# Kernel optimization log

Hardware: AMD Instinct MI355X
Metric: run time of the kernel (lower is better)

The kernel has to match this reference:

```python
import jax, jax.numpy as jnp
import numpy as np


def _rope(xh, theta_factor):
    # xh: [H, S, Dqk]; rotate first half against second half (as in source)
    S, D = xh.shape[-2], xh.shape[-1]
    d_rope = D // 2
    rate = theta_factor * (-jnp.arange(0, d_rope, dtype=xh.dtype) / d_rope)
    pos = jnp.arange(0, S, dtype=xh.dtype)
    rot = pos[:, None] * rate[None, :]            # [S, d_rope]
    sin, cos = jnp.sin(rot), jnp.cos(rot)
    x1, x2 = xh[..., :d_rope], xh[..., d_rope:]
    y1 = cos * x1 - sin * x2
    y2 = sin * x1 + cos * x2
    return jnp.concatenate([y1, y2], axis=-1)


def _mha(x, y, q, k, v, o, theta_factor):
    S = x.shape[0]
    d_model = x.shape[1]
    x_scale = 1.0 / jnp.sqrt(jnp.array(x.shape[1], x.dtype))
    y_scale = 1.0 / jnp.sqrt(jnp.array(y.shape[1], x.dtype))
    # causal additive mask: 0 on/below diagonal, -1e9 above
    mask = (jnp.tril(jnp.ones((S, S), x.dtype)) - 1.0) * 1000000000.0
    # per-head projections (note: source uses x_scale for both q and k)
    pre_q = jnp.einsum('sd,hdk->hsk', x, q) * x_scale
    pre_k = jnp.einsum('td,hdk->htk', y, k) * x_scale
    vs = jnp.einsum('td,hdv->htv', y, v) * y_scale
    rq = _rope(pre_q, theta_factor)
    rk = _rope(pre_k, theta_factor)
    attn_scale = 1.0 / jnp.sqrt(jnp.array(rq.shape[-1], x.dtype))
    scores = jnp.einsum('hsk,htk->hst', rq, rk) * attn_scale + mask
    w = jax.nn.softmax(scores, axis=-1)           # [H, S, S]
    z = jnp.einsum('hst,htv->hsv', w, vs)         # [H, S, Dv]
    out_scale = 1.0 / jnp.sqrt(jnp.array(o.shape[0] * o.shape[1], x.dtype))
    return jnp.einsum('hsv,hvd->sd', z, o) * out_scale


def setup_inputs() -> dict:
    key = jax.random.key(0)
    ks = jax.random.split(key, 5)
    S, D, H, Dqk, Dv = 2048, 2048, 16, 128, 128
    return {
        'x': jax.random.normal(ks[0], (S, D), jnp.float32),
        'q': jax.random.normal(ks[1], (H, D, Dqk), jnp.float32),
        'k': jax.random.normal(ks[2], (H, D, Dqk), jnp.float32),
        'v': jax.random.normal(ks[3], (H, D, Dv), jnp.float32),
        'o': jax.random.normal(ks[4], (H, Dv, D), jnp.float32),
        'theta_factor': jnp.array(10000.0, jnp.float32),
    }


def reference(x, q, k, v, o, theta_factor):
    # self-attention path (y = x), scale = 1
    return _mha(x, x, q, k, v, o, theta_factor)
```

## Files before the change

kernel.cpp:

```cpp
#include <hip/hip_runtime.h>


#define S_LEN   2048
#define D_MODEL 2048
#define NHEAD   16
#define DHEAD   128

using f32x4   = __attribute__((ext_vector_type(4))) float;
using f32x16  = __attribute__((ext_vector_type(16))) float;
using bf16x8  = __attribute__((ext_vector_type(8))) __bf16;

__device__ __forceinline__ unsigned short f2bf(float f) {
  unsigned int u = __builtin_bit_cast(unsigned int, f);
  u += 0x7fffu + ((u >> 16) & 1u);
  return (unsigned short)(u >> 16);
}
__device__ __forceinline__ int chunks_of(int qt) { return (4 * qt + 13) / 10; }

__device__ __forceinline__ void gl_lds16(const unsigned short* g, char* l) {
  __builtin_amdgcn_global_load_lds(
      (const __attribute__((address_space(1))) unsigned int*)g,
      (__attribute__((address_space(3))) unsigned int*)l, 16, 0, 0);
}

__global__ void k_cvt(const float* __restrict__ in, unsigned short* __restrict__ out) {
  int i = (blockIdx.x * 256 + threadIdx.x) * 4;
  float4 v = *reinterpret_cast<const float4*>(in + i);
  ushort4 o; o.x = f2bf(v.x); o.y = f2bf(v.y); o.z = f2bf(v.z); o.w = f2bf(v.w);
  *reinterpret_cast<ushort4*>(out + i) = o;
}

__global__ void k_tab(const float* __restrict__ theta_p, float* __restrict__ sint,
                      float* __restrict__ cost) {
  int i = blockIdx.x * 256 + threadIdx.x;
  int s = i >> 6, c = i & 63;
  float rate = theta_p[0] * (-(float)c / 64.0f);
  float sn, cs;
  sincosf((float)s * rate, &sn, &cs);
  sint[i] = sn; cost[i] = cs;
}

__global__ void k_tr(const float* __restrict__ in, unsigned short* __restrict__ out,
                     int R, int C) {
  __shared__ float t[32][33];
  int b = blockIdx.x, rt = blockIdx.y, ct = blockIdx.z;
  const float* ip = in + (size_t)b * R * C;
  unsigned short* op = out + (size_t)b * R * C;
  int tx = threadIdx.x & 31, ty = threadIdx.x >> 5;
  #pragma unroll
  for (int i = 0; i < 4; i++)
    t[ty + i * 8][tx] = ip[(size_t)(rt * 32 + ty + i * 8) * C + ct * 32 + tx];
  __syncthreads();
  #pragma unroll
  for (int i = 0; i < 4; i++)
    op[(size_t)(ct * 32 + ty + i * 8) * R + rt * 32 + tx] = f2bf(t[tx][ty + i * 8]);
}

__global__ __launch_bounds__(256) void k_proj2(
    const unsigned short* __restrict__ xb, const unsigned short* __restrict__ wT,
    const float* __restrict__ sint, const float* __restrict__ cost,
    unsigned short* __restrict__ rq, unsigned short* __restrict__ rk,
    unsigned short* __restrict__ vst) {
  __shared__ char lds[65536];
  const int tid = threadIdx.x, l = tid & 63, w = tid >> 6;
  const int lr = l & 15, lk = l >> 4;
  const int orig = blockIdx.x;
  const int wg = (orig & 7) * 96 + (orig >> 3);
  const int bx = wg & 15, by = wg >> 4;
  const int s0 = bx * 128;
  const int h = by & 15, which = by >> 4;
  const unsigned short* bbase = wT + (size_t)by * 128 * D_MODEL;

  f32x4 acc[2][8] = {};

  auto stage = [&](int t, int buf) {
    const int kt = t * 64;
    char* dst = lds + buf * 32768;
    #pragma unroll
    for (int j = 0; j < 4; j++) {
      int ci = (j * 4 + w) * 64 + l;
      int r = ci >> 3, c8 = ci & 7;
      int csrc = (c8 ^ (r & 7)) * 8;
      gl_lds16(xb + (size_t)(s0 + r) * D_MODEL + kt + csrc, dst + ci * 16);
      gl_lds16(bbase + (size_t)r * D_MODEL + kt + csrc, dst + 16384 + ci * 16);
    }
  };

  stage(0, 0);
  int cur = 0;
  const int nT = D_MODEL / 64;
  for (int t = 0; t < nT; t++) {
    if (t + 1 < nT) {
      stage(t + 1, cur ^ 1);
      asm volatile("s_waitcnt vmcnt(8)" ::: "memory");
    } else {
      asm volatile("s_waitcnt vmcnt(0)" ::: "memory");
    }
    __builtin_amdgcn_s_barrier();
    const char* base = lds + cur * 32768;
    #pragma unroll
    for (int kk = 0; kk < 2; kk++) {
      const int kb = kk * 64 + lk * 16;
      bf16x8 a[2], b[8];
      #pragma unroll
      for (int mf = 0; mf < 2; mf++) {
        int rr = w * 32 + mf * 16 + lr;
        a[mf] = *reinterpret_cast<const bf16x8*>(base + rr * 128 + (kb ^ ((rr & 7) << 4)));
      }
      #pragma unroll
      for (int nf = 0; nf < 8; nf++) {
        int rn = nf * 16 + lr;
        b[nf] = *reinterpret_cast<const bf16x8*>(base + 16384 + rn * 128 + (kb ^ ((rn & 7) << 4)));
      }
      #pragma unroll
      for (int mf = 0; mf < 2; mf++)
        #pragma unroll
        for (int nf = 0; nf < 8; nf++)
          acc[mf][nf] = __builtin_amdgcn_mfma_f32_16x16x32_bf16(a[mf], b[nf], acc[mf][nf], 0, 0, 0);
    }
    asm volatile("s_waitcnt lgkmcnt(0)" ::: "memory");
    __builtin_amdgcn_s_barrier();
    cur ^= 1;
  }

  const float xscale = 0.022097086912079608f;
  const float qsc = xscale * 0.08838834764831845f;
  if (which < 2) {
    const float sc_out = (which == 0) ? qsc : xscale;
    unsigned short* dst = (which == 0 ? rq : rk) + (size_t)h * S_LEN * DHEAD;
    #pragma unroll
    for (int mf = 0; mf < 2; mf++) {
      #pragma unroll
      for (int nf = 0; nf < 4; nf++) {
        int c1 = nf * 16 + lr;
        #pragma unroll
        for (int rg = 0; rg < 4; rg++) {
          int srow = s0 + w * 32 + mf * 16 + lk * 4 + rg;
          float sn = sint[srow * 64 + c1], cs = cost[srow * 64 + c1];
          float x1 = acc[mf][nf][rg] * sc_out;
          float x2 = acc[mf][nf + 4][rg] * sc_out;
          dst[(size_t)srow * DHEAD + c1]      = f2bf(cs * x1 - sn * x2);
          dst[(size_t)srow * DHEAD + c1 + 64] = f2bf(sn * x1 + cs * x2);
        }
      }
    }
  } else {
    unsigned short* dst = vst + (size_t)h * DHEAD * S_LEN;
    #pragma unroll
    for (int mf = 0; mf < 2; mf++) {
      int rbase = s0 + w * 32 + mf * 16 + lk * 4;
      #pragma unroll
      for (int nf = 0; nf < 8; nf++) {
        int c = nf * 16 + lr;
        ushort4 ov;
        ov.x = f2bf(acc[mf][nf][0] * xscale); ov.y = f2bf(acc[mf][nf][1] * xscale);
        ov.z = f2bf(acc[mf][nf][2] * xscale); ov.w = f2bf(acc[mf][nf][3] * xscale);
        *reinterpret_cast<ushort4*>(dst + (size_t)c * S_LEN + rbase) = ov;
      }
    }
  }
}

__global__ __launch_bounds__(256, 2) void k_attn6(
    const unsigned short* __restrict__ rq, const unsigned short* __restrict__ rk,
    const unsigned short* __restrict__ vst,
    unsigned short* __restrict__ opart, float2* __restrict__ mlbuf) {
  __shared__ uint4 ldsbuf[2368];
  char* lds = (char*)ldsbuf;
  const int tid = threadIdx.x, l = tid & 63, w = tid >> 6;
  const int hi = l >> 5, qcol = l & 31;
  const int b = blockIdx.x;
  const int h = b & 15;
  int u = b >> 4, qt = 0;
  while (u >= chunks_of(qt)) { u -= chunks_of(qt); qt++; }
  const int ntile = 4 * qt + 4;
  const int tbeg = u * 10;
  const int tend = (tbeg + 10 < ntile) ? tbeg + 10 : ntile;
  const int s0w = qt * 128 + w * 32;
  const int wlast = s0w + 31;
  const int dtile = s0w >> 5;

  const unsigned short* rk_h  = rk  + (size_t)h * S_LEN * DHEAD;
  const unsigned short* vst_h = vst + (size_t)h * DHEAD * S_LEN;

  const unsigned short* qrow_p = rq + ((size_t)h * S_LEN + s0w + qcol) * DHEAD + hi * 8;
  bf16x8 qb[8];
  #pragma unroll
  for (int kk = 0; kk < 8; kk++)
    qb[kk] = *reinterpret_cast<const bf16x8*>(qrow_p + kk * 16);

  f32x16 O[4] = {};
  float mrow = -3.0e38f, lrow = 0.0f;

  uint4 kreg[2], vreg[2];
  auto ld_regs = [&](int t) {
    const int t0 = t * 32;
    #pragma unroll
    for (int j = 0; j < 2; j++) {
      int ci = tid + j * 256;
      kreg[j] = *reinterpret_cast<const uint4*>(rk_h + (size_t)(t0 + (ci >> 4)) * DHEAD + (ci & 15) * 8);
      vreg[j] = *reinterpret_cast<const uint4*>(vst_h + (size_t)(ci >> 2) * S_LEN + t0 + (ci & 3) * 8);
    }
  };
  auto wr_lds = [&](int p) {
    char* dst = lds + p * 18944;
    #pragma unroll
    for (int j = 0; j < 2; j++) {
      int ci = tid + j * 256;
      *reinterpret_cast<uint4*>(dst + (ci >> 4) * 272 + (ci & 15) * 16) = kreg[j];
      *reinterpret_cast<uint4*>(dst + 8704 + (ci >> 2) * 80 + (ci & 3) * 16) = vreg[j];
    }
  };

  ld_regs(tbeg);
  wr_lds(0);
  if (tbeg + 1 < tend) ld_regs(tbeg + 1);
  asm volatile("s_waitcnt lgkmcnt(0)" ::: "memory");
  __builtin_amdgcn_s_barrier();

  int cur = 0;
  for (int t = tbeg; t < tend; t++) {
    const char* kb = lds + cur * 18944;
    const char* vb = kb + 8704;
    const int tt0 = t * 32;
    if (tt0 <= wlast) {
      f32x16 sc = {};
      #pragma unroll
      for (int kk = 0; kk < 8; kk++) {
        bf16x8 ka = *reinterpret_cast<const bf16x8*>(kb + qcol * 272 + kk * 32 + hi * 16);
        sc = __builtin_amdgcn_mfma_f32_32x32x16_bf16(ka, qb[kk], sc, 0, 0, 0);
      }
      float p[16];
      #pragma unroll
      for (int r = 0; r < 16; r++) p[r] = sc[r];
      if (t == dtile) {
        #pragma unroll
        for (int r = 0; r < 16; r++)
          if (((r & 3) + 8 * (r >> 2) + 4 * hi) > qcol) p[r] = -1.0e9f;
      }
      float mx[8];
      #pragma unroll
      for (int i = 0; i < 8; i++) mx[i] = fmaxf(p[2 * i], p[2 * i + 1]);
      #pragma unroll
      for (int i = 0; i < 4; i++) mx[i] = fmaxf(mx[i], mx[i + 4]);
      mx[0] = fmaxf(mx[0], mx[2]); mx[1] = fmaxf(mx[1], mx[3]);
      float pmax = fmaxf(mx[0], mx[1]);
      pmax = fmaxf(pmax, __shfl_xor(pmax, 32, 64));
      if (__any(pmax > mrow + 8.0f)) {
        float mn = fmaxf(mrow, pmax);
        float sf = __expf(mrow - mn);
        lrow *= sf; mrow = mn;
        #pragma unroll
        for (int vc = 0; vc < 4; vc++)
          #pragma unroll
          for (int r = 0; r < 16; r++) O[vc][r] *= sf;
      }
      #pragma unroll
      for (int r = 0; r < 16; r++) p[r] = __expf(p[r] - mrow);
      float sm[8];
      #pragma unroll
      for (int i = 0; i < 8; i++) sm[i] = p[2 * i] + p[2 * i + 1];
      #pragma unroll
      for (int i = 0; i < 4; i++) sm[i] += sm[i + 4];
      float psum = (sm[0] + sm[1]) + (sm[2] + sm[3]);
      psum += __shfl_xor(psum, 32, 64);
      lrow += psum;
      unsigned int pk[2][4], sw[2][4];
      #pragma unroll
      for (int c = 0; c < 2; c++)
        #pragma unroll
        for (int k = 0; k < 4; k++) {
          unsigned int r_;
          asm("v_cvt_pk_bf16_f32 %0, %1, %2" : "=v"(r_)
              : "v"(p[8 * c + 2 * k]), "v"(p[8 * c + 2 * k + 1]));
          pk[c][k] = r_;
          sw[c][k] = (unsigned int)__shfl_xor((int)r_, 32, 64);
        }
      bf16x8 pb[2];
      #pragma unroll
      for (int c = 0; c < 2; c++) {
        union { unsigned int u4[4]; bf16x8 v; } bw;
        bw.u4[0] = hi ? sw[c][2] : pk[c][0];
        bw.u4[1] = hi ? sw[c][3] : pk[c][1];
        bw.u4[2] = hi ? pk[c][2] : sw[c][0];
        bw.u4[3] = hi ? pk[c][3] : sw[c][1];
        pb[c] = bw.v;
      }
      #pragma unroll
      for (int vc = 0; vc < 4; vc++) {
        const char* vrow = vb + (vc * 32 + qcol) * 80 + hi * 16;
        bf16x8 va0 = *reinterpret_cast<const bf16x8*>(vrow);
        bf16x8 va1 = *reinterpret_cast<const bf16x8*>(vrow + 32);
        O[vc] = __builtin_amdgcn_mfma_f32_32x32x16_bf16(va0, pb[0], O[vc], 0, 0, 0);
        O[vc] = __builtin_amdgcn_mfma_f32_32x32x16_bf16(va1, pb[1], O[vc], 0, 0, 0);
      }
    }
    if (t + 1 < tend) {
      wr_lds(cur ^ 1);
      if (t + 2 < tend) ld_regs(t + 2);
    }
    asm volatile("s_waitcnt lgkmcnt(0)" ::: "memory");
    __builtin_amdgcn_s_barrier();
    cur ^= 1;
  }

  __syncthreads();
  float inv = lrow > 0.0f ? 1.0f / lrow : 0.0f;
  #pragma unroll
  for (int vc = 0; vc < 4; vc++)
    #pragma unroll
    for (int g = 0; g < 4; g++) {
      int v0 = vc * 32 + 8 * g + 4 * hi;
      ushort4 ov;
      ov.x = f2bf(O[vc][4 * g + 0] * inv); ov.y = f2bf(O[vc][4 * g + 1] * inv);
      ov.z = f2bf(O[vc][4 * g + 2] * inv); ov.w = f2bf(O[vc][4 * g + 3] * inv);
      *reinterpret_cast<ushort4*>(lds + (w * 32 + qcol) * 272 + v0 * 2) = ov;
    }
  __syncthreads();
  #pragma unroll
  for (int j = 0; j < 8; j++) {
    int row = w * 32 + j * 4 + (l >> 4);
    uint4 vv = *reinterpret_cast<const uint4*>(lds + row * 272 + (l & 15) * 16);
    *reinterpret_cast<uint4*>(opart + ((size_t)b * 128 + row) * DHEAD + (l & 15) * 8) = vv;
  }
  if (l < 32)
    mlbuf[(size_t)b * 128 + w * 32 + l] = make_float2(mrow, lrow);
}

__global__ void k_comb2(const unsigned short* __restrict__ opart,
                        const float2* __restrict__ mlbuf,
                        unsigned short* __restrict__ z) {
  int g = blockIdx.x * 256 + threadIdx.x;
  int vg = g & 15, q = (g >> 4) & 2047, h = g >> 15;
  int qt = q >> 7, r = q & 127;
  int base = 0;
  for (int j = 0; j < qt; j++) base += chunks_of(j);
  const int nc = chunks_of(qt);
  float m = -3.0e38f;
  float2 ml[7];
  #pragma unroll
  for (int cc = 0; cc < 7; cc++)
    if (cc < nc) {
      ml[cc] = mlbuf[(size_t)((base + cc) * 16 + h) * 128 + r];
      m = fmaxf(m, ml[cc].x);
    }
  float wts[7], wsum = 0.0f;
  #pragma unroll
  for (int cc = 0; cc < 7; cc++)
    if (cc < nc) {
      float wv = ml[cc].y > 0.0f ? ml[cc].y * __expf(ml[cc].x - m) : 0.0f;
      wts[cc] = wv; wsum += wv;
    }
  float wi = 1.0f / wsum;
  float acc[8] = {};
  #pragma unroll
  for (int cc = 0; cc < 7; cc++)
    if (cc < nc && wts[cc] > 0.0f) {
      float wv = wts[cc] * wi;
      bf16x8 v = *reinterpret_cast<const bf16x8*>(
          opart + ((size_t)((base + cc) * 16 + h) * 128 + r) * DHEAD + vg * 8);
      #pragma unroll
      for (int j = 0; j < 8; j++) acc[j] += wv * (float)v[j];
    }
  unsigned short* zp = z + (size_t)q * D_MODEL + h * DHEAD + vg * 8;
  ushort4 lo, hi4;
  lo.x = f2bf(acc[0]); lo.y = f2bf(acc[1]); lo.z = f2bf(acc[2]); lo.w = f2bf(acc[3]);
  hi4.x = f2bf(acc[4]); hi4.y = f2bf(acc[5]); hi4.z = f2bf(acc[6]); hi4.w = f2bf(acc[7]);
  *reinterpret_cast<ushort4*>(zp) = lo;
  *reinterpret_cast<ushort4*>(zp + 4) = hi4;
}

__global__ __launch_bounds__(256) void k_out2(
    const unsigned short* __restrict__ zb, const unsigned short* __restrict__ obT,
    float* __restrict__ out) {
  __shared__ char lds[65536];
  const int tid = threadIdx.x, l = tid & 63, w = tid >> 6;
  const int lr = l & 15, lk = l >> 4;
  const int orig = blockIdx.x;
  const int wg = (orig & 7) * 32 + (orig >> 3);
  const int bx = wg & 15, by = wg >> 4;
  const int s0 = bx * 128, n0 = by * 128;
  const int wm = w >> 1, wn = w & 1;
  f32x4 acc[4][4] = {};

  auto stage = [&](int t, int buf) {
    const int kt = t * 64;
    char* dst = lds + buf * 32768;
    #pragma unroll
    for (int j = 0; j < 4; j++) {
      int ci = (j * 4 + w) * 64 + l;
      int r = ci >> 3, c8 = ci & 7;
      int csrc = (c8 ^ (r & 7)) * 8;
      gl_lds16(zb + (size_t)(s0 + r) * D_MODEL + kt + csrc, dst + ci * 16);
      gl_lds16(obT + (size_t)(n0 + r) * D_MODEL + kt + csrc, dst + 16384 + ci * 16);
    }
  };

  stage(0, 0);
  int cur = 0;
  const int nT = D_MODEL / 64;
  for (int t = 0; t < nT; t++) {
    if (t + 1 < nT) {
      stage(t + 1, cur ^ 1);
      asm volatile("s_waitcnt vmcnt(8)" ::: "memory");
    } else {
      asm volatile("s_waitcnt vmcnt(0)" ::: "memory");
    }
    __builtin_amdgcn_s_barrier();
    const char* base = lds + cur * 32768;
    #pragma unroll
    for (int kk = 0; kk < 2; kk++) {
      const int kb = kk * 64 + lk * 16;
      bf16x8 a[4], b[4];
      #pragma unroll
      for (int mf = 0; mf < 4; mf++) {
        int rr = wm * 64 + mf * 16 + lr;
        a[mf] = *reinterpret_cast<const bf16x8*>(base + rr * 128 + (kb ^ ((rr & 7) << 4)));
      }
      #pragma unroll
      for (int nf = 0; nf < 4; nf++) {
        int rn = wn * 64 + nf * 16 + lr;
        b[nf] = *reinterpret_cast<const bf16x8*>(base + 16384 + rn * 128 + (kb ^ ((rn & 7) << 4)));
      }
      #pragma unroll
      for (int mf = 0; mf < 4; mf++)
        #pragma unroll
        for (int nf = 0; nf < 4; nf++)
          acc[mf][nf] = __builtin_amdgcn_mfma_f32_16x16x32_bf16(a[mf], b[nf], acc[mf][nf], 0, 0, 0);
    }
    asm volatile("s_waitcnt lgkmcnt(0)" ::: "memory");
    __builtin_amdgcn_s_barrier();
    cur ^= 1;
  }
  const float osc = 0.022097086912079608f;
  #pragma unroll
  for (int mf = 0; mf < 4; mf++)
    #pragma unroll
    for (int nf = 0; nf < 4; nf++)
      #pragma unroll
      for (int rg = 0; rg < 4; rg++)
        out[(size_t)(s0 + wm * 64 + mf * 16 + lk * 4 + rg) * D_MODEL + n0 + wn * 64 + nf * 16 + lr]
            = acc[mf][nf][rg] * osc;
}

extern "C" void kernel_launch(void* const* d_in, const int* in_sizes, int n_in,
                              void* d_out, int out_size, void* d_ws, size_t ws_size,
                              hipStream_t stream) {
  const float* x = (const float*)d_in[0];
  const float* q = (const float*)d_in[1];
  const float* k = (const float*)d_in[2];
  const float* v = (const float*)d_in[3];
  const float* o = (const float*)d_in[4];
  const float* theta = (const float*)d_in[5];
  float* out = (float*)d_out;

  char* ws = (char*)d_ws;
  const size_t MB = 1u << 20;
  unsigned short* xb  = (unsigned short*)(ws + 0 * MB);
  unsigned short* qbT = (unsigned short*)(ws + 8 * MB);
  unsigned short* kbT = (unsigned short*)(ws + 16 * MB);
  unsigned short* vbT = (unsigned short*)(ws + 24 * MB);
  unsigned short* obT = (unsigned short*)(ws + 32 * MB);
  unsigned short* rq  = (unsigned short*)(ws + 40 * MB);
  unsigned short* rk  = (unsigned short*)(ws + 48 * MB);
  unsigned short* vst = (unsigned short*)(ws + 56 * MB);
  float* sint = (float*)(ws + 64 * MB);
  float* cost = (float*)(ws + 64 * MB + 512 * 1024);
  unsigned short* opart = (unsigned short*)(ws + 0 * MB);
  float2* mlbuf         = (float2*)(ws + 31 * MB);
  unsigned short* zb    = (unsigned short*)(ws + 40 * MB);

  k_cvt<<<dim3(4096), dim3(256), 0, stream>>>(x, xb);
  k_tab<<<dim3(512), dim3(256), 0, stream>>>(theta, sint, cost);
  k_tr<<<dim3(16, 64, 4), dim3(256), 0, stream>>>(q, qbT, 2048, 128);
  k_tr<<<dim3(16, 64, 4), dim3(256), 0, stream>>>(k, kbT, 2048, 128);
  k_tr<<<dim3(16, 64, 4), dim3(256), 0, stream>>>(v, vbT, 2048, 128);
  k_tr<<<dim3(1, 64, 64), dim3(256), 0, stream>>>(o, obT, 2048, 2048);
  k_proj2<<<dim3(768), dim3(256), 0, stream>>>(xb, qbT, sint, cost, rq, rk, vst);
  k_attn6<<<dim3(976), dim3(256), 0, stream>>>(rq, rk, vst, opart, mlbuf);
  k_comb2<<<dim3(2048), dim3(256), 0, stream>>>(opart, mlbuf, zb);
  k_out2<<<dim3(256), dim3(256), 0, stream>>>(zb, obT, out);
}
```

Baseline: 192.1 us.

## Fuse prep kernels into one launch, shrink proj K-tile, split out-proj M tile

Six preprocessing launches (x conversion, sin/cos table, four weight transposes) are merged into one k_prep kernel that dispatches on block index, cutting launch overhead and tail gaps. The QKV projection GEMM now uses a 32-wide K tile with a 4-chunk swizzle and half the LDS, which may allow more resident blocks per CU but doubles the barrier count. The output GEMM tile shrinks from 128x128 to 64x128, giving 512 blocks instead of 256 to fill more CUs, at the cost of more redundant weight loads.

```diff
diff --git a/kernel.cpp b/kernel.cpp
--- a/kernel.cpp
+++ b/kernel.cpp
@@ -23,37 +23,50 @@
       (__attribute__((address_space(3))) unsigned int*)l, 16, 0, 0);
 }
 
-__global__ void k_cvt(const float* __restrict__ in, unsigned short* __restrict__ out) {
-  int i = (blockIdx.x * 256 + threadIdx.x) * 4;
-  float4 v = *reinterpret_cast<const float4*>(in + i);
-  ushort4 o; o.x = f2bf(v.x); o.y = f2bf(v.y); o.z = f2bf(v.z); o.w = f2bf(v.w);
-  *reinterpret_cast<ushort4*>(out + i) = o;
-}
-
-__global__ void k_tab(const float* __restrict__ theta_p, float* __restrict__ sint,
-                      float* __restrict__ cost) {
-  int i = blockIdx.x * 256 + threadIdx.x;
-  int s = i >> 6, c = i & 63;
-  float rate = theta_p[0] * (-(float)c / 64.0f);
-  float sn, cs;
-  sincosf((float)s * rate, &sn, &cs);
-  sint[i] = sn; cost[i] = cs;
-}
-
-__global__ void k_tr(const float* __restrict__ in, unsigned short* __restrict__ out,
-                     int R, int C) {
+__global__ __launch_bounds__(256) void k_prep(
+    const float* __restrict__ x, const float* __restrict__ q,
+    const float* __restrict__ k, const float* __restrict__ v,
+    const float* __restrict__ o, const float* __restrict__ theta_p,
+    unsigned short* __restrict__ xb, unsigned short* __restrict__ wT,
+    unsigned short* __restrict__ obT, float* __restrict__ sint,
+    float* __restrict__ cost) {
   __shared__ float t[32][33];
-  int b = blockIdx.x, rt = blockIdx.y, ct = blockIdx.z;
-  const float* ip = in + (size_t)b * R * C;
-  unsigned short* op = out + (size_t)b * R * C;
-  int tx = threadIdx.x & 31, ty = threadIdx.x >> 5;
-  #pragma unroll
-  for (int i = 0; i < 4; i++)
-    t[ty + i * 8][tx] = ip[(size_t)(rt * 32 + ty + i * 8) * C + ct * 32 + tx];
-  __syncthreads();
-  #pragma unroll
-  for (int i = 0; i < 4; i++)
-    op[(size_t)(ct * 32 + ty + i * 8) * R + rt * 32 + tx] = f2bf(t[tx][ty + i * 8]);
+  const int bid = blockIdx.x, tid = threadIdx.x;
+  if (bid < 4096) {
+    int i = (bid * 256 + tid) * 4;
+    float4 vv = *reinterpret_cast<const float4*>(x + i);
+    ushort4 ov; ov.x = f2bf(vv.x); ov.y = f2bf(vv.y); ov.z = f2bf(vv.z); ov.w = f2bf(vv.w);
+    *reinterpret_cast<ushort4*>(xb + i) = ov;
+  } else if (bid < 4608) {
+    int i = (bid - 4096) * 256 + tid;
+    int s = i >> 6, c = i & 63;
+    float rate = theta_p[0] * (-(float)c / 64.0f);
+    float sn, cs;
+    sincosf((float)s * rate, &sn, &cs);
+    sint[i] = sn; cost[i] = cs;
+  } else {
+    int ti = bid - 4608;
+    int which = ti >> 12, i = ti & 4095;
+    const float* ip; unsigned short* op; int C, b, rt, ct;
+    const int R = 2048;
+    if (which < 3) {
+      C = 128; b = i >> 8; rt = (i >> 2) & 63; ct = i & 3;
+      const float* src = which == 0 ? q : (which == 1 ? k : v);
+      ip = src + (size_t)b * R * C;
+      op = wT + (size_t)which * 4194304 + (size_t)b * R * C;
+    } else {
+      C = 2048; rt = i >> 6; ct = i & 63;
+      ip = o; op = obT;
+    }
+    int tx = tid & 31, ty = tid >> 5;
+    #pragma unroll
+    for (int j = 0; j < 4; j++)
+      t[ty + j * 8][tx] = ip[(size_t)(rt * 32 + ty + j * 8) * C + ct * 32 + tx];
+    __syncthreads();
+    #pragma unroll
+    for (int j = 0; j < 4; j++)
+      op[(size_t)(ct * 32 + ty + j * 8) * R + rt * 32 + tx] = f2bf(t[tx][ty + j * 8]);
+  }
 }
 
 __global__ __launch_bounds__(256) void k_proj2(
@@ -61,7 +74,7 @@
     const float* __restrict__ sint, const float* __restrict__ cost,
     unsigned short* __restrict__ rq, unsigned short* __restrict__ rk,
     unsigned short* __restrict__ vst) {
-  __shared__ char lds[65536];
+  __shared__ char lds[32768];
   const int tid = threadIdx.x, l = tid & 63, w = tid >> 6;
   const int lr = l & 15, lk = l >> 4;
   const int orig = blockIdx.x;
@@ -74,50 +87,46 @@
   f32x4 acc[2][8] = {};
 
   auto stage = [&](int t, int buf) {
-    const int kt = t * 64;
-    char* dst = lds + buf * 32768;
-    #pragma unroll
-    for (int j = 0; j < 4; j++) {
-      int ci = (j * 4 + w) * 64 + l;
-      int r = ci >> 3, c8 = ci & 7;
-      int csrc = (c8 ^ (r & 7)) * 8;
+    const int kt = t * 32;
+    char* dst = lds + buf * 16384;
+    #pragma unroll
+    for (int j = 0; j < 2; j++) {
+      int ci = tid + j * 256;
+      int r = ci >> 2, c4 = ci & 3;
+      int csrc = (c4 ^ ((r >> 1) & 3)) * 8;
       gl_lds16(xb + (size_t)(s0 + r) * D_MODEL + kt + csrc, dst + ci * 16);
-      gl_lds16(bbase + (size_t)r * D_MODEL + kt + csrc, dst + 16384 + ci * 16);
+      gl_lds16(bbase + (size_t)r * D_MODEL + kt + csrc, dst + 8192 + ci * 16);
     }
   };
 
   stage(0, 0);
   int cur = 0;
-  const int nT = D_MODEL / 64;
+  const int nT = D_MODEL / 32;
   for (int t = 0; t < nT; t++) {
     if (t + 1 < nT) {
       stage(t + 1, cur ^ 1);
-      asm volatile("s_waitcnt vmcnt(8)" ::: "memory");
+      asm volatile("s_waitcnt vmcnt(4)" ::: "memory");
     } else {
       asm volatile("s_waitcnt vmcnt(0)" ::: "memory");
     }
     __builtin_amdgcn_s_barrier();
-    const char* base = lds + cur * 32768;
-    #pragma unroll
-    for (int kk = 0; kk < 2; kk++) {
-      const int kb = kk * 64 + lk * 16;
-      bf16x8 a[2], b[8];
-      #pragma unroll
-      for (int mf = 0; mf < 2; mf++) {
-        int rr = w * 32 + mf * 16 + lr;
-        a[mf] = *reinterpret_cast<const bf16x8*>(base + rr * 128 + (kb ^ ((rr & 7) << 4)));
-      }
-      #pragma unroll
-      for (int nf = 0; nf < 8; nf++) {
-        int rn = nf * 16 + lr;
-        b[nf] = *reinterpret_cast<const bf16x8*>(base + 16384 + rn * 128 + (kb ^ ((rn & 7) << 4)));
-      }
-      #pragma unroll
-      for (int mf = 0; mf < 2; mf++)
-        #pragma unroll
-        for (int nf = 0; nf < 8; nf++)
-          acc[mf][nf] = __builtin_amdgcn_mfma_f32_16x16x32_bf16(a[mf], b[nf], acc[mf][nf], 0, 0, 0);
-    }
+    const char* base = lds + cur * 16384;
+    bf16x8 a[2], b[8];
+    #pragma unroll
+    for (int mf = 0; mf < 2; mf++) {
+      int rr = w * 32 + mf * 16 + lr;
+      a[mf] = *reinterpret_cast<const bf16x8*>(base + rr * 64 + ((lk ^ ((rr >> 1) & 3)) * 16));
+    }
+    #pragma unroll
+    for (int nf = 0; nf < 8; nf++) {
+      int rn = nf * 16 + lr;
+      b[nf] = *reinterpret_cast<const bf16x8*>(base + 8192 + rn * 64 + ((lk ^ ((rn >> 1) & 3)) * 16));
+    }
+    #pragma unroll
+    for (int mf = 0; mf < 2; mf++)
+      #pragma unroll
+      for (int nf = 0; nf < 8; nf++)
+        acc[mf][nf] = __builtin_amdgcn_mfma_f32_16x16x32_bf16(a[mf], b[nf], acc[mf][nf], 0, 0, 0);
     asm volatile("s_waitcnt lgkmcnt(0)" ::: "memory");
     __builtin_amdgcn_s_barrier();
     cur ^= 1;
@@ -373,26 +382,32 @@
 __global__ __launch_bounds__(256) void k_out2(
     const unsigned short* __restrict__ zb, const unsigned short* __restrict__ obT,
     float* __restrict__ out) {
-  __shared__ char lds[65536];
+  __shared__ char lds[49152];
   const int tid = threadIdx.x, l = tid & 63, w = tid >> 6;
   const int lr = l & 15, lk = l >> 4;
   const int orig = blockIdx.x;
-  const int wg = (orig & 7) * 32 + (orig >> 3);
-  const int bx = wg & 15, by = wg >> 4;
-  const int s0 = bx * 128, n0 = by * 128;
+  const int wg = (orig & 7) * 64 + (orig >> 3);
+  const int bx = wg & 31, by = wg >> 5;
+  const int s0 = bx * 64, n0 = by * 128;
   const int wm = w >> 1, wn = w & 1;
-  f32x4 acc[4][4] = {};
+  f32x4 acc[2][4] = {};
 
   auto stage = [&](int t, int buf) {
     const int kt = t * 64;
-    char* dst = lds + buf * 32768;
-    #pragma unroll
-    for (int j = 0; j < 4; j++) {
-      int ci = (j * 4 + w) * 64 + l;
+    char* dst = lds + buf * 24576;
+    #pragma unroll
+    for (int j = 0; j < 2; j++) {
+      int ci = tid + j * 256;
       int r = ci >> 3, c8 = ci & 7;
       int csrc = (c8 ^ (r & 7)) * 8;
       gl_lds16(zb + (size_t)(s0 + r) * D_MODEL + kt + csrc, dst + ci * 16);
-      gl_lds16(obT + (size_t)(n0 + r) * D_MODEL + kt + csrc, dst + 16384 + ci * 16);
+    }
+    #pragma unroll
+    for (int j = 0; j < 4; j++) {
+      int ci = tid + j * 256;
+      int r = ci >> 3, c8 = ci & 7;
+      int csrc = (c8 ^ (r & 7)) * 8;
+      gl_lds16(obT + (size_t)(n0 + r) * D_MODEL + kt + csrc, dst + 8192 + ci * 16);
     }
   };
 
@@ -402,28 +417,28 @@
   for (int t = 0; t < nT; t++) {
     if (t + 1 < nT) {
       stage(t + 1, cur ^ 1);
-      asm volatile("s_waitcnt vmcnt(8)" ::: "memory");
+      asm volatile("s_waitcnt vmcnt(6)" ::: "memory");
     } else {
       asm volatile("s_waitcnt vmcnt(0)" ::: "memory");
     }
     __builtin_amdgcn_s_barrier();
-    const char* base = lds + cur * 32768;
+    const char* base = lds + cur * 24576;
     #pragma unroll
     for (int kk = 0; kk < 2; kk++) {
       const int kb = kk * 64 + lk * 16;
-      bf16x8 a[4], b[4];
-      #pragma unroll
-      for (int mf = 0; mf < 4; mf++) {
-        int rr = wm * 64 + mf * 16 + lr;
+      bf16x8 a[2], b[4];
+      #pragma unroll
+      for (int mf = 0; mf < 2; mf++) {
+        int rr = wm * 32 + mf * 16 + lr;
         a[mf] = *reinterpret_cast<const bf16x8*>(base + rr * 128 + (kb ^ ((rr & 7) << 4)));
       }
       #pragma unroll
       for (int nf = 0; nf < 4; nf++) {
         int rn = wn * 64 + nf * 16 + lr;
-        b[nf] = *reinterpret_cast<const bf16x8*>(base + 16384 + rn * 128 + (kb ^ ((rn & 7) << 4)));
-      }
-      #pragma unroll
-      for (int mf = 0; mf < 4; mf++)
+        b[nf] = *reinterpret_cast<const bf16x8*>(base + 8192 + rn * 128 + (kb ^ ((rn & 7) << 4)));
+      }
+      #pragma unroll
+      for (int mf = 0; mf < 2; mf++)
         #pragma unroll
         for (int nf = 0; nf < 4; nf++)
           acc[mf][nf] = __builtin_amdgcn_mfma_f32_16x16x32_bf16(a[mf], b[nf], acc[mf][nf], 0, 0, 0);
@@ -434,12 +449,12 @@
   }
   const float osc = 0.022097086912079608f;
   #pragma unroll
-  for (int mf = 0; mf < 4; mf++)
+  for (int mf = 0; mf < 2; mf++)
     #pragma unroll
     for (int nf = 0; nf < 4; nf++)
       #pragma unroll
       for (int rg = 0; rg < 4; rg++)
-        out[(size_t)(s0 + wm * 64 + mf * 16 + lk * 4 + rg) * D_MODEL + n0 + wn * 64 + nf * 16 + lr]
+        out[(size_t)(s0 + wm * 32 + mf * 16 + lk * 4 + rg) * D_MODEL + n0 + wn * 64 + nf * 16 + lr]
             = acc[mf][nf][rg] * osc;
 }
 
@@ -458,8 +473,6 @@
   const size_t MB = 1u << 20;
   unsigned short* xb  = (unsigned short*)(ws + 0 * MB);
   unsigned short* qbT = (unsigned short*)(ws + 8 * MB);
-  unsigned short* kbT = (unsigned short*)(ws + 16 * MB);
-  unsigned short* vbT = (unsigned short*)(ws + 24 * MB);
   unsigned short* obT = (unsigned short*)(ws + 32 * MB);
   unsigned short* rq  = (unsigned short*)(ws + 40 * MB);
   unsigned short* rk  = (unsigned short*)(ws + 48 * MB);
@@ -470,14 +483,9 @@
   float2* mlbuf         = (float2*)(ws + 31 * MB);
   unsigned short* zb    = (unsigned short*)(ws + 40 * MB);
 
-  k_cvt<<<dim3(4096), dim3(256), 0, stream>>>(x, xb);
-  k_tab<<<dim3(512), dim3(256), 0, stream>>>(theta, sint, cost);
-  k_tr<<<dim3(16, 64, 4), dim3(256), 0, stream>>>(q, qbT, 2048, 128);
-  k_tr<<<dim3(16, 64, 4), dim3(256), 0, stream>>>(k, kbT, 2048, 128);
-  k_tr<<<dim3(16, 64, 4), dim3(256), 0, stream>>>(v, vbT, 2048, 128);
-  k_tr<<<dim3(1, 64, 64), dim3(256), 0, stream>>>(o, obT, 2048, 2048);
+  k_prep<<<dim3(20992), dim3(256), 0, stream>>>(x, q, k, v, o, theta, xb, qbT, obT, sint, cost);
   k_proj2<<<dim3(768), dim3(256), 0, stream>>>(xb, qbT, sint, cost, rq, rk, vst);
   k_attn6<<<dim3(976), dim3(256), 0, stream>>>(rq, rk, vst, opart, mlbuf);
   k_comb2<<<dim3(2048), dim3(256), 0, stream>>>(opart, mlbuf, zb);
-  k_out2<<<dim3(256), dim3(256), 0, stream>>>(zb, obT, out);
-}
+  k_out2<<<dim3(512), dim3(256), 0, stream>>>(zb, obT, out);
+}
```

Result: faster. 180.4 us (-6.1%).
